# Optimization experiments

Hardware: AMD Instinct MI355X
Metric: run time of the kernel (lower is better)

## Reference

```python
import jax, jax.numpy as jnp
import numpy as np

NUM_HEADS = 4
HEAD_DIM = 128  # out_dim // num_heads = 512 // 4
TOP_K = 16
NEG_SLOPE = 0.2


def setup_inputs() -> dict:
    key = jax.random.key(0)
    k1, k2, k3, k4 = jax.random.split(key, 4)
    N, in_dim, out_dim = 4096, 1024, 512
    x = jax.random.normal(k1, (N, in_dim), dtype=jnp.float32)
    adj = jax.random.uniform(k2, (N, N), dtype=jnp.float32)  # all-positive, like softmax attn
    W = jax.random.normal(k3, (out_dim, in_dim), dtype=jnp.float32) * 0.02
    a = jax.random.normal(k4, (1, 2 * HEAD_DIM), dtype=jnp.float32) * 0.02
    return {"x": x, "adj": adj, "W": W, "a": a}


def reference(x, adj, W, a):
    N = x.shape[0]
    Wh = (x @ W.T).reshape(N, NUM_HEADS, HEAD_DIM)  # (N, H, D)

    # _sparsify_adj: keep top-k per row, binary mask
    k = min(TOP_K, N)
    _, topk_idx = jax.lax.top_k(adj, k)  # (N, k)
    rows = jnp.arange(N)[:, None]
    sparse = jnp.zeros_like(adj).at[rows, topk_idx].set(1.0)
    mask = sparse > 0  # (N_i, N_j)

    # a([Wh_i, Wh_j]) decomposed: a = [a_src | a_dst], score = s_i + s_j
    a_src, a_dst = a[0, :HEAD_DIM], a[0, HEAD_DIM:]
    s_i = jnp.einsum("nhd,d->nh", Wh, a_src)  # (N, H)
    s_j = jnp.einsum("nhd,d->nh", Wh, a_dst)  # (N, H)
    e = jax.nn.leaky_relu(s_i[:, None, :] + s_j[None, :, :], NEG_SLOPE)  # (N_i, N_j, H)
    e = jnp.where(mask[:, :, None], e, -jnp.inf)

    alpha = jax.nn.softmax(e, axis=1)  # softmax over neighbors j
    alpha = jnp.nan_to_num(alpha, nan=0.0)

    out = jnp.einsum("imh,mhd->ihd", alpha, Wh)  # weighted sum over j
    return jax.nn.elu(out.reshape(N, -1))  # (N, out_dim)
```

## Files before the change

kernel.cpp:

```cpp
#include <hip/hip_runtime.h>
#include <hip/hip_bf16.h>

#define N_NODES 4096
#define IN_DIM 1024
#define OUT_DIM 512
#define NUM_HEADS 4
#define HEAD_DIM 128
#define TOP_K 16
#define NEG_SLOPE 0.2f

typedef __attribute__((ext_vector_type(8))) short bf16x8;
typedef __attribute__((ext_vector_type(4))) float f32x4;

typedef __attribute__((address_space(3))) unsigned as3_u32;
typedef const __attribute__((address_space(1))) unsigned as1_u32;

static __device__ __forceinline__ void gld16(const void* g, void* l) {
    __builtin_amdgcn_global_load_lds((as1_u32*)g, (as3_u32*)l, 16, 0, 0);
}

__device__ __forceinline__ unsigned short f2bf(float f) {
    unsigned u = __float_as_uint(f);
    unsigned r = u + 0x7FFFu + ((u >> 16) & 1u);
    return (unsigned short)(r >> 16);
}
__device__ __forceinline__ float bf2f(unsigned short h) {
    return __uint_as_float(((unsigned)h) << 16);
}

__device__ __forceinline__ void conv_row(const float* __restrict__ src,
                                         unsigned short* __restrict__ dst, int t)
{
    int row = t >> 7, rem = t & 127, kb = rem >> 2, c = rem & 3;
    const float* s = src + (size_t)row * IN_DIM + kb * 32 + c * 8;
    float4 v0 = *(const float4*)s;
    float4 v1 = *(const float4*)(s + 4);
    float vv[8] = {v0.x, v0.y, v0.z, v0.w, v1.x, v1.y, v1.z, v1.w};
    bf16x8 H, L;
#pragma unroll
    for (int e = 0; e < 8; ++e) {
        unsigned short h = f2bf(vv[e]);
        H[e] = (short)h;
        L[e] = (short)f2bf(vv[e] - bf2f(h));
    }
    int sw = row & 7;
    unsigned short* base = dst + (size_t)row * 2048 + kb * 64;
    *(bf16x8*)(base + ((c ^ sw) << 3))       = H;
    *(bf16x8*)(base + (((c + 4) ^ sw) << 3)) = L;
}

__global__ __launch_bounds__(256) void prep_kernel(
    const float* __restrict__ x, const float* __restrict__ W,
    unsigned short* __restrict__ xc, unsigned short* __restrict__ wc,
    float* __restrict__ szero)
{
    int b = blockIdx.x, tid = threadIdx.x;
    if (b < 2048) {
        conv_row(x, xc, b * 256 + tid);
    } else if (b < 2304) {
        conv_row(W, wc, (b - 2048) * 256 + tid);
    } else {
        int t = (b - 2304) * 256 + tid;
        ((float4*)szero)[t] = (float4){0.f, 0.f, 0.f, 0.f};
    }
}

#define GBM 64
#define GBN 64

__global__ __launch_bounds__(256) void gemm_kernel(
    const unsigned short* __restrict__ xc, const unsigned short* __restrict__ wc,
    const float* __restrict__ a, float* __restrict__ Wh,
    float* __restrict__ s_src, float* __restrict__ s_dst)
{
    __shared__ __align__(16) unsigned short A0[GBM * 64];
    __shared__ __align__(16) unsigned short A1[GBM * 64];
    __shared__ __align__(16) unsigned short A2[GBM * 64];
    __shared__ __align__(16) unsigned short B0[GBN * 64];
    __shared__ __align__(16) unsigned short B1[GBN * 64];
    __shared__ __align__(16) unsigned short B2[GBN * 64];

    const int tid = threadIdx.x;
    const int id  = blockIdx.x;
    const int xcd = id & 7, seq = id >> 3;
    const int bm  = xcd * 8 + (seq >> 3), bn = seq & 7;

    const int wn = tid >> 6, lane = tid & 63;
    const int lr = lane & 15, lk = lane >> 4;

    f32x4 acc[4];
#pragma unroll
    for (int i = 0; i < 4; ++i) acc[i] = (f32x4){0.f, 0.f, 0.f, 0.f};

#define STAGE(Abuf, Bbuf, kt) do {                                            \
        size_t koff = (size_t)(kt) * 128;                                     \
        _Pragma("unroll")                                                     \
        for (int q = 0; q < 2; ++q) {                                         \
            int ci = q * 256 + tid;                                           \
            int row = ci >> 3, p = ci & 7;                                    \
            gld16((const char*)xc + ((size_t)(bm * GBM + row) * 4096 + koff + p * 16), \
                  (char*)(Abuf) + (size_t)ci * 16);                           \
            gld16((const char*)wc + ((size_t)(bn * GBN + row) * 4096 + koff + p * 16), \
                  (char*)(Bbuf) + (size_t)ci * 16);                           \
        }                                                                     \
    } while (0)

#define COMPUTE(Abuf, Bbuf) do {                                              \
        int rb = wn * 16 + lr; int swb = rb & 7;                              \
        bf16x8 bh = *(const bf16x8*)&(Bbuf)[rb * 64 + ((lk ^ swb) << 3)];     \
        bf16x8 bl = *(const bf16x8*)&(Bbuf)[rb * 64 + (((4 + lk) ^ swb) << 3)]; \
        __builtin_amdgcn_s_setprio(1);                                        \
        _Pragma("unroll")                                                     \
        for (int mi = 0; mi < 4; ++mi) {                                      \
            int r = mi * 16 + lr; int sw = r & 7;                             \
            bf16x8 ah = *(const bf16x8*)&(Abuf)[r * 64 + ((lk ^ sw) << 3)];   \
            bf16x8 al = *(const bf16x8*)&(Abuf)[r * 64 + (((4 + lk) ^ sw) << 3)]; \
            acc[mi] = __builtin_amdgcn_mfma_f32_16x16x32_bf16(ah, bh, acc[mi], 0, 0, 0); \
            acc[mi] = __builtin_amdgcn_mfma_f32_16x16x32_bf16(ah, bl, acc[mi], 0, 0, 0); \
            acc[mi] = __builtin_amdgcn_mfma_f32_16x16x32_bf16(al, bh, acc[mi], 0, 0, 0); \
        }                                                                     \
        __builtin_amdgcn_s_setprio(0);                                        \
    } while (0)

#define BODY(Ac, Bc, An, Bn, ktn, W) do {                                     \
        asm volatile("s_waitcnt vmcnt(" #W ")" ::: "memory");                 \
        __builtin_amdgcn_s_barrier();                                         \
        asm volatile("" ::: "memory");                                        \
        if ((ktn) < 32) STAGE(An, Bn, ktn);                                   \
        COMPUTE(Ac, Bc);                                                      \
    } while (0)

    STAGE(A0, B0, 0);
    STAGE(A1, B1, 1);

    for (int i = 0; i < 10; ++i) {
        int t = i * 3;
        BODY(A0, B0, A2, B2, t + 2, 4);
        BODY(A1, B1, A0, B0, t + 3, 4);
        BODY(A2, B2, A1, B1, t + 4, 4);
    }
    BODY(A0, B0, A2, B2, 32, 4);
    asm volatile("s_waitcnt vmcnt(0)" ::: "memory");
    __builtin_amdgcn_s_barrier();
    asm volatile("" ::: "memory");
    COMPUTE(A1, B1);

#undef BODY
#undef COMPUTE
#undef STAGE

    const int col_g = bn * GBN + wn * 16 + lr;
    const int h = col_g >> 7, d = col_g & (HEAD_DIM - 1);
    const float ca = a[d], cb = a[HEAD_DIM + d];
#pragma unroll
    for (int mi = 0; mi < 4; ++mi) {
        float ss[4], sd[4];
#pragma unroll
        for (int r = 0; r < 4; ++r) {
            int row_g = bm * GBM + mi * 16 + lk * 4 + r;
            float v = acc[mi][r];
            Wh[(size_t)row_g * OUT_DIM + col_g] = v;
            ss[r] = v * ca;
            sd[r] = v * cb;
        }
#pragma unroll
        for (int s = 1; s < 16; s <<= 1)
#pragma unroll
            for (int r = 0; r < 4; ++r) {
                ss[r] += __shfl_xor(ss[r], s);
                sd[r] += __shfl_xor(sd[r], s);
            }
        if (lr == 0) {
#pragma unroll
            for (int r = 0; r < 4; ++r) {
                int row_g = bm * GBM + mi * 16 + lk * 4 + r;
                atomicAdd(&s_src[row_g * NUM_HEADS + h], ss[r]);
                atomicAdd(&s_dst[row_g * NUM_HEADS + h], sd[r]);
            }
        }
    }
}

#define TK_THRESH 0.988f
#define TK_CAP 128

__global__ __launch_bounds__(256) void topk_kernel(
    const float* __restrict__ adj, int* __restrict__ topk)
{
    const int wave = threadIdx.x >> 6, lane = threadIdx.x & 63;
    const int row  = blockIdx.x * 4 + wave;
    const float* rp = adj + (size_t)row * N_NODES;
    __shared__ unsigned long long cand[4][TK_CAP];

    float v[64];
#pragma unroll
    for (int i = 0; i < 16; ++i) {
        float4 q = *(const float4*)(rp + i * 256 + lane * 4);
        v[i * 4 + 0] = q.x; v[i * 4 + 1] = q.y; v[i * 4 + 2] = q.z; v[i * 4 + 3] = q.w;
    }
    int* op = topk + (size_t)row * TOP_K;

    const unsigned long long lmask = (1ull << lane) - 1ull;
    int cnt = 0;
#pragma unroll
    for (int s = 0; s < 64; ++s) {
        int g = (s >> 2) * 256 + lane * 4 + (s & 3);
        bool p = v[s] >= TK_THRESH;
        unsigned long long m = __ballot(p);
        if (p) {
            int pos = cnt + __popcll(m & lmask);
            if (pos < TK_CAP) {
                unsigned b  = __float_as_uint(v[s]);
                unsigned mo = b ^ (unsigned)(((int)b >> 31) | 0x80000000);
                cand[wave][pos] =
                    ((unsigned long long)mo << 32) | (unsigned)(N_NODES - 1 - g);
            }
        }
        cnt += __popcll(m);
    }

    if (cnt >= TOP_K && cnt <= TK_CAP) {
        for (int j = cnt + lane; j < TK_CAP; j += 64) cand[wave][j] = 0ull;
        unsigned long long c0 = cand[wave][lane], c1 = cand[wave][lane + 64];
        for (int r = 0; r < TOP_K; ++r) {
            unsigned long long b = c0 > c1 ? c0 : c1;
#pragma unroll
            for (int m = 1; m < 64; m <<= 1) {
                unsigned long long o = __shfl_xor(b, m);
                b = o > b ? o : b;
            }
            if (lane == 0) op[r] = N_NODES - 1 - (int)(unsigned)(b & 0xFFFFFFFFu);
            if (c0 == b) c0 = 0ull;
            if (c1 == b) c1 = 0ull;
        }
    } else {
        for (int r = 0; r < TOP_K; ++r) {
            float bv = -INFINITY; int bg = 0x7fffffff;
#pragma unroll
            for (int s = 0; s < 64; ++s) {
                int g = (s >> 2) * 256 + lane * 4 + (s & 3);
                bool better = (v[s] > bv) || (v[s] == bv && g < bg);
                bv = better ? v[s] : bv;
                bg = better ? g : bg;
            }
#pragma unroll
            for (int m = 1; m < 64; m <<= 1) {
                float ov = __shfl_xor(bv, m);
                int   og = __shfl_xor(bg, m);
                bool better = (ov > bv) || (ov == bv && og < bg);
                bv = better ? ov : bv;
                bg = better ? og : bg;
            }
            if (lane == 0) op[r] = bg;
#pragma unroll
            for (int s = 0; s < 64; ++s) {
                int g = (s >> 2) * 256 + lane * 4 + (s & 3);
                if (g == bg) v[s] = -INFINITY;
            }
        }
    }
}

__global__ __launch_bounds__(256) void aggregate_kernel(
    const float* __restrict__ Wh, const int* __restrict__ topk,
    const float* __restrict__ s_src, const float* __restrict__ s_dst,
    float* __restrict__ out)
{
    const int i = blockIdx.x, t = threadIdx.x;
    __shared__ int   sidx[TOP_K];
    __shared__ float salpha[TOP_K][NUM_HEADS];
    __shared__ float4 part[128];

    if (t < 64) {
        int idxv = 0;
        if (t < TOP_K) { idxv = topk[(size_t)i * TOP_K + t]; sidx[t] = idxv; }
        int m = t >> 2, h = t & 3;
        int im = __shfl(idxv, m);
        float e = s_src[i * NUM_HEADS + h] + s_dst[im * NUM_HEADS + h];
        e = (e >= 0.f) ? e : NEG_SLOPE * e;
        float mx = e;
#pragma unroll
        for (int s = 4; s < 64; s <<= 1) mx = fmaxf(mx, __shfl_xor(mx, s));
        float ex = expf(e - mx);
        float sum = ex;
#pragma unroll
        for (int s = 4; s < 64; s <<= 1) sum += __shfl_xor(sum, s);
        salpha[m][h] = ex / sum;
    }
    __syncthreads();

    const int c4 = t & 127, half = t >> 7;
    const int h = c4 >> 5;
    float4 acc = (float4){0.f, 0.f, 0.f, 0.f};
#pragma unroll
    for (int mm = 0; mm < 8; ++mm) {
        int m = half * 8 + mm;
        float al = salpha[m][h];
        float4 v = *(const float4*)(Wh + (size_t)sidx[m] * OUT_DIM + c4 * 4);
        acc.x += al * v.x; acc.y += al * v.y;
        acc.z += al * v.z; acc.w += al * v.w;
    }
    if (half) part[c4] = acc;
    __syncthreads();
    if (!half) {
        float4 o = part[c4];
        acc.x += o.x; acc.y += o.y; acc.z += o.z; acc.w += o.w;
        float4 r;
        r.x = acc.x > 0.f ? acc.x : expf(acc.x) - 1.f;
        r.y = acc.y > 0.f ? acc.y : expf(acc.y) - 1.f;
        r.z = acc.z > 0.f ? acc.z : expf(acc.z) - 1.f;
        r.w = acc.w > 0.f ? acc.w : expf(acc.w) - 1.f;
        *(float4*)(out + (size_t)i * OUT_DIM + c4 * 4) = r;
    }
}

extern "C" void kernel_launch(void* const* d_in, const int* in_sizes, int n_in,
                              void* d_out, int out_size, void* d_ws, size_t ws_size,
                              hipStream_t stream) {
    const float* x   = (const float*)d_in[0];
    const float* adj = (const float*)d_in[1];
    const float* W   = (const float*)d_in[2];
    const float* a   = (const float*)d_in[3];
    float* out = (float*)d_out;

    char* ws = (char*)d_ws;
    float*          Wh    = (float*)ws;
    unsigned short* xc    = (unsigned short*)(ws + (8u << 20));
    unsigned short* wc    = (unsigned short*)(ws + (24u << 20));
    float*          s_src = (float*)(ws + (26u << 20));
    float*          s_dst = s_src + N_NODES * NUM_HEADS;
    int*            topkb = (int*)(s_dst + N_NODES * NUM_HEADS);

    prep_kernel<<<2336, 256, 0, stream>>>(x, W, xc, wc, s_src);
    gemm_kernel<<<512, 256, 0, stream>>>(xc, wc, a, Wh, s_src, s_dst);
    topk_kernel<<<N_NODES / 4, 256, 0, stream>>>(adj, topkb);
    aggregate_kernel<<<N_NODES, 256, 0, stream>>>(Wh, topkb, s_src, s_dst, out);
}
```

Baseline: 172.9 us.

## Enlarge GEMM M-tile to 128, store Wh as bf16, regroup aggregation

The GEMM block tile grows from 64x64 to 128x64, with a 2x2 wave layout and two N sub-tiles per wave. This doubles MFMA work per B-fragment load and halves the grid to 256 blocks. Wh is now written as bf16 instead of fp32, which halves its write traffic and the gather traffic in the aggregate kernel. The aggregate kernel reads 8 bf16 values per thread across four neighbor groups and does a 4-way shared-memory reduction. The costs are lower Wh precision, fewer blocks (the grid may underfill the CUs) and a larger LDS footprint.

```diff
diff --git a/kernel.cpp b/kernel.cpp
--- a/kernel.cpp
+++ b/kernel.cpp
@@ -65,12 +65,12 @@
     }
 }
 
-#define GBM 64
+#define GBM 128
 #define GBN 64
 
 __global__ __launch_bounds__(256) void gemm_kernel(
     const unsigned short* __restrict__ xc, const unsigned short* __restrict__ wc,
-    const float* __restrict__ a, float* __restrict__ Wh,
+    const float* __restrict__ a, unsigned short* __restrict__ Whb,
     float* __restrict__ s_src, float* __restrict__ s_dst)
 {
     __shared__ __align__(16) unsigned short A0[GBM * 64];
@@ -83,41 +83,56 @@
     const int tid = threadIdx.x;
     const int id  = blockIdx.x;
     const int xcd = id & 7, seq = id >> 3;
-    const int bm  = xcd * 8 + (seq >> 3), bn = seq & 7;
-
-    const int wn = tid >> 6, lane = tid & 63;
+    const int bm  = xcd * 4 + (seq >> 3), bn = seq & 7;
+
+    const int wave = tid >> 6, lane = tid & 63;
+    const int wm = wave >> 1, wn = wave & 1;
     const int lr = lane & 15, lk = lane >> 4;
 
-    f32x4 acc[4];
-#pragma unroll
-    for (int i = 0; i < 4; ++i) acc[i] = (f32x4){0.f, 0.f, 0.f, 0.f};
+    f32x4 acc[4][2];
+#pragma unroll
+    for (int i = 0; i < 4; ++i)
+#pragma unroll
+        for (int j = 0; j < 2; ++j) acc[i][j] = (f32x4){0.f, 0.f, 0.f, 0.f};
 
 #define STAGE(Abuf, Bbuf, kt) do {                                            \
         size_t koff = (size_t)(kt) * 128;                                     \
         _Pragma("unroll")                                                     \
-        for (int q = 0; q < 2; ++q) {                                         \
+        for (int q = 0; q < 4; ++q) {             \
             int ci = q * 256 + tid;                                           \
             int row = ci >> 3, p = ci & 7;                                    \
             gld16((const char*)xc + ((size_t)(bm * GBM + row) * 4096 + koff + p * 16), \
                   (char*)(Abuf) + (size_t)ci * 16);                           \
+        }                                                                     \
+        _Pragma("unroll")                                                     \
+        for (int q = 0; q < 2; ++q) {               \
+            int ci = q * 256 + tid;                                           \
+            int row = ci >> 3, p = ci & 7;                                    \
             gld16((const char*)wc + ((size_t)(bn * GBN + row) * 4096 + koff + p * 16), \
                   (char*)(Bbuf) + (size_t)ci * 16);                           \
         }                                                                     \
     } while (0)
 
 #define COMPUTE(Abuf, Bbuf) do {                                              \
-        int rb = wn * 16 + lr; int swb = rb & 7;                              \
-        bf16x8 bh = *(const bf16x8*)&(Bbuf)[rb * 64 + ((lk ^ swb) << 3)];     \
-        bf16x8 bl = *(const bf16x8*)&(Bbuf)[rb * 64 + (((4 + lk) ^ swb) << 3)]; \
+        bf16x8 bh[2], bl[2];                                                  \
+        _Pragma("unroll")                                                     \
+        for (int ni = 0; ni < 2; ++ni) {                                      \
+            int rb = wn * 32 + ni * 16 + lr; int swb = rb & 7;                \
+            bh[ni] = *(const bf16x8*)&(Bbuf)[rb * 64 + ((lk ^ swb) << 3)];    \
+            bl[ni] = *(const bf16x8*)&(Bbuf)[rb * 64 + (((4 + lk) ^ swb) << 3)]; \
+        }                                                                     \
         __builtin_amdgcn_s_setprio(1);                                        \
         _Pragma("unroll")                                                     \
         for (int mi = 0; mi < 4; ++mi) {                                      \
-            int r = mi * 16 + lr; int sw = r & 7;                             \
+            int r = wm * 64 + mi * 16 + lr; int sw = r & 7;                   \
             bf16x8 ah = *(const bf16x8*)&(Abuf)[r * 64 + ((lk ^ sw) << 3)];   \
             bf16x8 al = *(const bf16x8*)&(Abuf)[r * 64 + (((4 + lk) ^ sw) << 3)]; \
-            acc[mi] = __builtin_amdgcn_mfma_f32_16x16x32_bf16(ah, bh, acc[mi], 0, 0, 0); \
-            acc[mi] = __builtin_amdgcn_mfma_f32_16x16x32_bf16(ah, bl, acc[mi], 0, 0, 0); \
-            acc[mi] = __builtin_amdgcn_mfma_f32_16x16x32_bf16(al, bh, acc[mi], 0, 0, 0); \
+            _Pragma("unroll")                                                 \
+            for (int ni = 0; ni < 2; ++ni) {                                  \
+                acc[mi][ni] = __builtin_amdgcn_mfma_f32_16x16x32_bf16(ah, bh[ni], acc[mi][ni], 0, 0, 0); \
+                acc[mi][ni] = __builtin_amdgcn_mfma_f32_16x16x32_bf16(ah, bl[ni], acc[mi][ni], 0, 0, 0); \
+                acc[mi][ni] = __builtin_amdgcn_mfma_f32_16x16x32_bf16(al, bh[ni], acc[mi][ni], 0, 0, 0); \
+            }                                                                 \
         }                                                                     \
         __builtin_amdgcn_s_setprio(0);                                        \
     } while (0)
@@ -135,11 +150,11 @@
 
     for (int i = 0; i < 10; ++i) {
         int t = i * 3;
-        BODY(A0, B0, A2, B2, t + 2, 4);
-        BODY(A1, B1, A0, B0, t + 3, 4);
-        BODY(A2, B2, A1, B1, t + 4, 4);
-    }
-    BODY(A0, B0, A2, B2, 32, 4);
+        BODY(A0, B0, A2, B2, t + 2, 6);
+        BODY(A1, B1, A0, B0, t + 3, 6);
+        BODY(A2, B2, A1, B1, t + 4, 6);
+    }
+    BODY(A0, B0, A2, B2, 32, 6);
     asm volatile("s_waitcnt vmcnt(0)" ::: "memory");
     __builtin_amdgcn_s_barrier();
     asm volatile("" ::: "memory");
@@ -149,19 +164,28 @@
 #undef COMPUTE
 #undef STAGE
 
-    const int col_g = bn * GBN + wn * 16 + lr;
-    const int h = col_g >> 7, d = col_g & (HEAD_DIM - 1);
-    const float ca = a[d], cb = a[HEAD_DIM + d];
+    const int h = bn >> 1;
+    float ca[2], cb[2];
+#pragma unroll
+    for (int ni = 0; ni < 2; ++ni) {
+        int dcol = (bn & 1) * 64 + wn * 32 + ni * 16 + lr;
+        ca[ni] = a[dcol];
+        cb[ni] = a[HEAD_DIM + dcol];
+    }
 #pragma unroll
     for (int mi = 0; mi < 4; ++mi) {
-        float ss[4], sd[4];
-#pragma unroll
-        for (int r = 0; r < 4; ++r) {
-            int row_g = bm * GBM + mi * 16 + lk * 4 + r;
-            float v = acc[mi][r];
-            Wh[(size_t)row_g * OUT_DIM + col_g] = v;
-            ss[r] = v * ca;
-            sd[r] = v * cb;
+        float ss[4] = {0.f, 0.f, 0.f, 0.f}, sd[4] = {0.f, 0.f, 0.f, 0.f};
+#pragma unroll
+        for (int ni = 0; ni < 2; ++ni) {
+            int col_g = bn * GBN + wn * 32 + ni * 16 + lr;
+#pragma unroll
+            for (int r = 0; r < 4; ++r) {
+                int row_g = bm * GBM + wm * 64 + mi * 16 + lk * 4 + r;
+                float v = acc[mi][ni][r];
+                Whb[(size_t)row_g * OUT_DIM + col_g] = f2bf(v);
+                ss[r] += v * ca[ni];
+                sd[r] += v * cb[ni];
+            }
         }
 #pragma unroll
         for (int s = 1; s < 16; s <<= 1)
@@ -173,7 +197,7 @@
         if (lr == 0) {
 #pragma unroll
             for (int r = 0; r < 4; ++r) {
-                int row_g = bm * GBM + mi * 16 + lk * 4 + r;
+                int row_g = bm * GBM + wm * 64 + mi * 16 + lk * 4 + r;
                 atomicAdd(&s_src[row_g * NUM_HEADS + h], ss[r]);
                 atomicAdd(&s_dst[row_g * NUM_HEADS + h], sd[r]);
             }
@@ -262,14 +286,14 @@
 }
 
 __global__ __launch_bounds__(256) void aggregate_kernel(
-    const float* __restrict__ Wh, const int* __restrict__ topk,
+    const unsigned short* __restrict__ Whb, const int* __restrict__ topk,
     const float* __restrict__ s_src, const float* __restrict__ s_dst,
     float* __restrict__ out)
 {
     const int i = blockIdx.x, t = threadIdx.x;
     __shared__ int   sidx[TOP_K];
     __shared__ float salpha[TOP_K][NUM_HEADS];
-    __shared__ float4 part[128];
+    __shared__ float part[3][8][64];
 
     if (t < 64) {
         int idxv = 0;
@@ -289,28 +313,34 @@
     }
     __syncthreads();
 
-    const int c4 = t & 127, half = t >> 7;
-    const int h = c4 >> 5;
-    float4 acc = (float4){0.f, 0.f, 0.f, 0.f};
-#pragma unroll
-    for (int mm = 0; mm < 8; ++mm) {
-        int m = half * 8 + mm;
+    const int g = t >> 6, o = t & 63;
+    const int h = o >> 4;
+    float acc8[8] = {0.f, 0.f, 0.f, 0.f, 0.f, 0.f, 0.f, 0.f};
+#pragma unroll
+    for (int q = 0; q < 4; ++q) {
+        int m = g * 4 + q;
         float al = salpha[m][h];
-        float4 v = *(const float4*)(Wh + (size_t)sidx[m] * OUT_DIM + c4 * 4);
-        acc.x += al * v.x; acc.y += al * v.y;
-        acc.z += al * v.z; acc.w += al * v.w;
-    }
-    if (half) part[c4] = acc;
+        bf16x8 v = *(const bf16x8*)&Whb[(size_t)sidx[m] * OUT_DIM + o * 8];
+#pragma unroll
+        for (int e = 0; e < 8; ++e)
+            acc8[e] += al * bf2f((unsigned short)v[e]);
+    }
+    if (g) {
+#pragma unroll
+        for (int e = 0; e < 8; ++e) part[g - 1][e][o] = acc8[e];
+    }
     __syncthreads();
-    if (!half) {
-        float4 o = part[c4];
-        acc.x += o.x; acc.y += o.y; acc.z += o.z; acc.w += o.w;
-        float4 r;
-        r.x = acc.x > 0.f ? acc.x : expf(acc.x) - 1.f;
-        r.y = acc.y > 0.f ? acc.y : expf(acc.y) - 1.f;
-        r.z = acc.z > 0.f ? acc.z : expf(acc.z) - 1.f;
-        r.w = acc.w > 0.f ? acc.w : expf(acc.w) - 1.f;
-        *(float4*)(out + (size_t)i * OUT_DIM + c4 * 4) = r;
+    if (!g) {
+        float r8[8];
+#pragma unroll
+        for (int e = 0; e < 8; ++e) {
+            float s = acc8[e] + part[0][e][o] + part[1][e][o] + part[2][e][o];
+            r8[e] = s > 0.f ? s : expf(s) - 1.f;
+        }
+        float4 lo = (float4){r8[0], r8[1], r8[2], r8[3]};
+        float4 hi = (float4){r8[4], r8[5], r8[6], r8[7]};
+        *(float4*)(out + (size_t)i * OUT_DIM + o * 8)     = lo;
+        *(float4*)(out + (size_t)i * OUT_DIM + o * 8 + 4) = hi;
     }
 }
 
@@ -324,7 +354,7 @@
     float* out = (float*)d_out;
 
     char* ws = (char*)d_ws;
-    float*          Wh    = (float*)ws;
+    unsigned short* Whb   = (unsigned short*)ws;
     unsigned short* xc    = (unsigned short*)(ws + (8u << 20));
     unsigned short* wc    = (unsigned short*)(ws + (24u << 20));
     float*          s_src = (float*)(ws + (26u << 20));
@@ -332,7 +362,7 @@
     int*            topkb = (int*)(s_dst + N_NODES * NUM_HEADS);
 
     prep_kernel<<<2336, 256, 0, stream>>>(x, W, xc, wc, s_src);
-    gemm_kernel<<<512, 256, 0, stream>>>(xc, wc, a, Wh, s_src, s_dst);
+    gemm_kernel<<<256, 256, 0, stream>>>(xc, wc, a, Whb, s_src, s_dst);
     topk_kernel<<<N_NODES / 4, 256, 0, stream>>>(adj, topkb);
-    aggregate_kernel<<<N_NODES, 256, 0, stream>>>(Wh, topkb, s_src, s_dst, out);
-}
+    aggregate_kernel<<<N_NODES, 256, 0, stream>>>(Whb, topkb, s_src, s_dst, out);
+}
```

Result: faster. 158.2 us (-8.5%).
